# Optimization experiments

Hardware: AMD Instinct MI355X
Metric: run time of the kernel (lower is better)

## Reference

```python
import jax, jax.numpy as jnp
import numpy as np

N0, N1, N2 = 409600, 40960, 4096
K = 10          # sampled fanout per dst node
IN, HID, NCLS = 512, 128, 64

def setup_inputs() -> dict:
    key = jax.random.key(0)
    ks = jax.random.split(key, 11)
    return {
        "embed":   jax.random.normal(ks[0], (N0, IN), jnp.float32),
        "h0_hist": jax.random.normal(ks[1], (N0, IN), jnp.float32),
        "h1_hist": jax.random.normal(ks[2], (N1, 2 * HID), jnp.float32),
        "agg_h0":  jax.random.normal(ks[3], (N1, IN), jnp.float32),
        "agg_h1":  jax.random.normal(ks[4], (N2, 2 * HID), jnp.float32),
        "W1": jax.random.normal(ks[5], (IN, HID), jnp.float32) / np.sqrt(IN),
        "b1": jax.random.normal(ks[6], (HID,), jnp.float32) * 0.01,
        "W2": jax.random.normal(ks[7], (2 * HID, NCLS), jnp.float32) / np.sqrt(2 * HID),
        "b2": jax.random.normal(ks[8], (NCLS,), jnp.float32) * 0.01,
        "nbr0": jax.random.randint(ks[9], (N1, K), 0, N0, jnp.int64),
        "nbr1": jax.random.randint(ks[10], (N2, K), 0, N1, jnp.int64),
    }

def reference(embed, h0_hist, h1_hist, agg_h0, agg_h1, W1, b1, W2, b2, nbr0, nbr1):
    # ---- block 0 (training branch): history correction + mean aggregation ----
    h = embed - h0_hist                      # [N0, IN]
    agg = jnp.mean(h[nbr0], axis=1)          # gather [N1, K, IN] -> mean -> [N1, IN]
    h = agg + agg_h0                         # add aggregated history (agg_h_0)
    h = h @ W1 + b1                          # dense [N1, HID]
    h = jnp.concatenate([h, jax.nn.relu(h)], axis=1)  # concat (skip_start) -> [N1, 2*HID]
    # ---- block 1: history correction + mean aggregation + final dense ----
    h = h - h1_hist                          # [N1, 2*HID]
    agg = jnp.mean(h[nbr1], axis=1)          # [N2, 2*HID]
    h = agg + agg_h1
    h = h @ W2 + b2                          # [N2, NCLS], no activation on last layer
    return h
```

## Files before the change

kernel.cpp:

```cpp
#include <hip/hip_runtime.h>
#include <stdint.h>

#define N0 409600
#define N1 40960
#define N2 4096
#define KF 10
#define IN 512
#define HID 128
#define NCLS 64
#define NB 16

static __device__ __forceinline__ float4 f4_zero() { return make_float4(0.f, 0.f, 0.f, 0.f); }

#define GATHER5x2(d0,d1,d2,d3,d4,d5,d6,d7,d8,d9, o0,o1,o2,o3,o4, base)      \
    asm volatile(                                                            \
        "global_load_dwordx4 %0, %10, %15 offset:0\n\t"                      \
        "global_load_dwordx4 %1, %10, %15 offset:16\n\t"                     \
        "global_load_dwordx4 %2, %11, %15 offset:0\n\t"                      \
        "global_load_dwordx4 %3, %11, %15 offset:16\n\t"                     \
        "global_load_dwordx4 %4, %12, %15 offset:0\n\t"                      \
        "global_load_dwordx4 %5, %12, %15 offset:16\n\t"                     \
        "global_load_dwordx4 %6, %13, %15 offset:0\n\t"                      \
        "global_load_dwordx4 %7, %13, %15 offset:16\n\t"                     \
        "global_load_dwordx4 %8, %14, %15 offset:0\n\t"                      \
        "global_load_dwordx4 %9, %14, %15 offset:16\n\t"                     \
        "s_waitcnt vmcnt(0)"                                                 \
        : "=&v"(d0), "=&v"(d1), "=&v"(d2), "=&v"(d3), "=&v"(d4),             \
          "=&v"(d5), "=&v"(d6), "=&v"(d7), "=&v"(d8), "=&v"(d9)              \
        : "v"(o0), "v"(o1), "v"(o2), "v"(o3), "v"(o4), "s"(base)             \
        : "memory")

#define GATHER10x1(d0,d1,d2,d3,d4,d5,d6,d7,d8,d9,                            \
                   o0,o1,o2,o3,o4,o5,o6,o7,o8,o9, base)                      \
    asm volatile(                                                            \
        "global_load_dwordx4 %0, %10, %20 offset:0\n\t"                      \
        "global_load_dwordx4 %1, %11, %20 offset:0\n\t"                      \
        "global_load_dwordx4 %2, %12, %20 offset:0\n\t"                      \
        "global_load_dwordx4 %3, %13, %20 offset:0\n\t"                      \
        "global_load_dwordx4 %4, %14, %20 offset:0\n\t"                      \
        "global_load_dwordx4 %5, %15, %20 offset:0\n\t"                      \
        "global_load_dwordx4 %6, %16, %20 offset:0\n\t"                      \
        "global_load_dwordx4 %7, %17, %20 offset:0\n\t"                      \
        "global_load_dwordx4 %8, %18, %20 offset:0\n\t"                      \
        "global_load_dwordx4 %9, %19, %20 offset:0\n\t"                      \
        "s_waitcnt vmcnt(0)"                                                 \
        : "=&v"(d0), "=&v"(d1), "=&v"(d2), "=&v"(d3), "=&v"(d4),             \
          "=&v"(d5), "=&v"(d6), "=&v"(d7), "=&v"(d8), "=&v"(d9)              \
        : "v"(o0), "v"(o1), "v"(o2), "v"(o3), "v"(o4),                       \
          "v"(o5), "v"(o6), "v"(o7), "v"(o8), "v"(o9), "s"(base)             \
        : "memory")

__global__ __launch_bounds__(256) void k_block0(
    const float* __restrict__ embed, const float* __restrict__ h0_hist,
    const float* __restrict__ h1_hist, const float* __restrict__ agg_h0,
    const float* __restrict__ W1, const float* __restrict__ b1,
    const int* __restrict__ nbr0, float* __restrict__ h1p)
{
    __shared__ float A[NB][IN];
    const int t = threadIdx.x;
    const int wave = t >> 6;
    const int lane = t & 63;
    const int base_node = blockIdx.x * NB;

    const uint64_t be = (uint64_t)embed;
    const uint64_t bg = (uint64_t)h0_hist;
    const uint32_t lane_byte = (uint32_t)lane * 32u;

    #pragma unroll 1
    for (int i = 0; i < NB / 4; ++i) {
        const int nl = wave * (NB / 4) + i;
        const int node = base_node + nl;
        const int nb = node * KF;
        float4 acc0 = f4_zero(), acc1 = f4_zero();

        int idx[KF];
        #pragma unroll
        for (int j = 0; j < KF; ++j) idx[j] = nbr0[nb + j];

        #pragma unroll 1
        for (int c = 0; c < 2; ++c) {
            uint32_t v0 = (uint32_t)idx[c * 5 + 0] * (uint32_t)(IN * 4) + lane_byte;
            uint32_t v1 = (uint32_t)idx[c * 5 + 1] * (uint32_t)(IN * 4) + lane_byte;
            uint32_t v2 = (uint32_t)idx[c * 5 + 2] * (uint32_t)(IN * 4) + lane_byte;
            uint32_t v3 = (uint32_t)idx[c * 5 + 3] * (uint32_t)(IN * 4) + lane_byte;
            uint32_t v4 = (uint32_t)idx[c * 5 + 4] * (uint32_t)(IN * 4) + lane_byte;

            float4 e0, e1, e2, e3, e4, e5, e6, e7, e8, e9;
            GATHER5x2(e0, e1, e2, e3, e4, e5, e6, e7, e8, e9,
                      v0, v1, v2, v3, v4, be);
            acc0.x += e0.x + e2.x + e4.x + e6.x + e8.x;
            acc0.y += e0.y + e2.y + e4.y + e6.y + e8.y;
            acc0.z += e0.z + e2.z + e4.z + e6.z + e8.z;
            acc0.w += e0.w + e2.w + e4.w + e6.w + e8.w;
            acc1.x += e1.x + e3.x + e5.x + e7.x + e9.x;
            acc1.y += e1.y + e3.y + e5.y + e7.y + e9.y;
            acc1.z += e1.z + e3.z + e5.z + e7.z + e9.z;
            acc1.w += e1.w + e3.w + e5.w + e7.w + e9.w;

            float4 g0, g1, g2, g3, g4, g5, g6, g7, g8, g9;
            GATHER5x2(g0, g1, g2, g3, g4, g5, g6, g7, g8, g9,
                      v0, v1, v2, v3, v4, bg);
            acc0.x -= g0.x + g2.x + g4.x + g6.x + g8.x;
            acc0.y -= g0.y + g2.y + g4.y + g6.y + g8.y;
            acc0.z -= g0.z + g2.z + g4.z + g6.z + g8.z;
            acc0.w -= g0.w + g2.w + g4.w + g6.w + g8.w;
            acc1.x -= g1.x + g3.x + g5.x + g7.x + g9.x;
            acc1.y -= g1.y + g3.y + g5.y + g7.y + g9.y;
            acc1.z -= g1.z + g3.z + g5.z + g7.z + g9.z;
            acc1.w -= g1.w + g3.w + g5.w + g7.w + g9.w;
        }

        const float s = 1.0f / (float)KF;
        const int col = lane * 8;
        const float4* ah = (const float4*)(agg_h0 + (size_t)node * IN + col);
        const float4 a0 = ah[0], a1 = ah[1];
        float4 r0, r1;
        r0.x = acc0.x * s + a0.x; r0.y = acc0.y * s + a0.y;
        r0.z = acc0.z * s + a0.z; r0.w = acc0.w * s + a0.w;
        r1.x = acc1.x * s + a1.x; r1.y = acc1.y * s + a1.y;
        r1.z = acc1.z * s + a1.z; r1.w = acc1.w * s + a1.w;
        *(float4*)&A[nl][col]     = r0;
        *(float4*)&A[nl][col + 4] = r1;
    }
    __syncthreads();

    const int c0 = (t & 31) * 4;
    const int rg = t >> 5;
    float4 acc[2];
    acc[0] = f4_zero(); acc[1] = f4_zero();

    #pragma unroll 4
    for (int k = 0; k < IN; ++k) {
        const float4 w = *(const float4*)&W1[k * HID + c0];
        #pragma unroll
        for (int i = 0; i < 2; ++i) {
            const float a = A[rg * 2 + i][k];
            acc[i].x += a * w.x; acc[i].y += a * w.y;
            acc[i].z += a * w.z; acc[i].w += a * w.w;
        }
    }

    const float4 bb = *(const float4*)&b1[c0];
    #pragma unroll
    for (int i = 0; i < 2; ++i) {
        const int node = base_node + rg * 2 + i;
        float4 h;
        h.x = acc[i].x + bb.x; h.y = acc[i].y + bb.y;
        h.z = acc[i].z + bb.z; h.w = acc[i].w + bb.w;
        const float4 hh0 = *(const float4*)&h1_hist[node * (2 * HID) + c0];
        const float4 hh1 = *(const float4*)&h1_hist[node * (2 * HID) + HID + c0];
        float4 o0, o1;
        o0.x = h.x - hh0.x; o0.y = h.y - hh0.y;
        o0.z = h.z - hh0.z; o0.w = h.w - hh0.w;
        o1.x = fmaxf(h.x, 0.f) - hh1.x; o1.y = fmaxf(h.y, 0.f) - hh1.y;
        o1.z = fmaxf(h.z, 0.f) - hh1.z; o1.w = fmaxf(h.w, 0.f) - hh1.w;
        *(float4*)&h1p[node * (2 * HID) + c0]       = o0;
        *(float4*)&h1p[node * (2 * HID) + HID + c0] = o1;
    }
}

__global__ __launch_bounds__(256) void k_block1(
    const float* __restrict__ h1p, const float* __restrict__ agg_h1,
    const float* __restrict__ W2, const float* __restrict__ b2,
    const int* __restrict__ nbr1, float* __restrict__ out)
{
    __shared__ float B[8][2 * HID + 4];
    const int t = threadIdx.x;
    const int wave = t >> 6;
    const int lane = t & 63;
    const int base_node = blockIdx.x * 8;
    const uint64_t bh = (uint64_t)h1p;
    const uint32_t lane_byte = (uint32_t)lane * 16u;

    #pragma unroll 1
    for (int i = 0; i < 2; ++i) {
        const int nl = wave * 2 + i;
        const int node = base_node + nl;
        const int nb = node * KF;

        uint32_t o[KF];
        #pragma unroll
        for (int j = 0; j < KF; ++j)
            o[j] = (uint32_t)nbr1[nb + j] * (uint32_t)(2 * HID * 4) + lane_byte;

        float4 v0, v1, v2, v3, v4, v5, v6, v7, v8, v9;
        GATHER10x1(v0, v1, v2, v3, v4, v5, v6, v7, v8, v9,
                   o[0], o[1], o[2], o[3], o[4],
                   o[5], o[6], o[7], o[8], o[9], bh);

        float4 acc;
        acc.x = v0.x + v1.x + v2.x + v3.x + v4.x + v5.x + v6.x + v7.x + v8.x + v9.x;
        acc.y = v0.y + v1.y + v2.y + v3.y + v4.y + v5.y + v6.y + v7.y + v8.y + v9.y;
        acc.z = v0.z + v1.z + v2.z + v3.z + v4.z + v5.z + v6.z + v7.z + v8.z + v9.z;
        acc.w = v0.w + v1.w + v2.w + v3.w + v4.w + v5.w + v6.w + v7.w + v8.w + v9.w;

        const float s = 1.0f / (float)KF;
        const int col = lane * 4;
        const float4 g = *(const float4*)&agg_h1[(size_t)node * (2 * HID) + col];
        float4 r;
        r.x = acc.x * s + g.x; r.y = acc.y * s + g.y;
        r.z = acc.z * s + g.z; r.w = acc.w * s + g.w;
        *(float4*)&B[nl][col] = r;
    }
    __syncthreads();

    const int r = t >> 5;
    const int c0 = (t & 31) * 2;
    float2 acc = make_float2(0.f, 0.f);
    #pragma unroll 4
    for (int k = 0; k < 2 * HID; ++k) {
        const float a = B[r][k];
        const float2 w = *(const float2*)&W2[k * NCLS + c0];
        acc.x += a * w.x; acc.y += a * w.y;
    }
    const float2 bb = *(const float2*)&b2[c0];
    float2 o;
    o.x = acc.x + bb.x; o.y = acc.y + bb.y;
    const int node = base_node + r;
    *(float2*)&out[node * NCLS + c0] = o;
}

extern "C" void kernel_launch(void* const* d_in, const int* in_sizes, int n_in,
                              void* d_out, int out_size, void* d_ws, size_t ws_size,
                              hipStream_t stream) {
    const float* embed   = (const float*)d_in[0];
    const float* h0_hist = (const float*)d_in[1];
    const float* h1_hist = (const float*)d_in[2];
    const float* agg_h0  = (const float*)d_in[3];
    const float* agg_h1  = (const float*)d_in[4];
    const float* W1      = (const float*)d_in[5];
    const float* b1      = (const float*)d_in[6];
    const float* W2      = (const float*)d_in[7];
    const float* b2      = (const float*)d_in[8];
    const int*   nbr0    = (const int*)d_in[9];
    const int*   nbr1    = (const int*)d_in[10];
    float* out = (float*)d_out;

    float* h1p = (float*)d_ws;

    k_block0<<<N1 / NB, 256, 0, stream>>>(embed, h0_hist, h1_hist, agg_h0,
                                          W1, b1, nbr0, h1p);
    k_block1<<<N2 / 8, 256, 0, stream>>>(h1p, agg_h1, W2, b2, nbr1, out);
}
```

Before: 442.4 us.

## Split block-0 gather and dense into separate kernels with wider gather batches

The fused block-0 kernel is split in two. A gather kernel handles one node per wave, issues all 20 embed and history loads for five neighbours in a single batch, and writes the aggregated rows to a workspace buffer. A separate dense kernel reloads those rows into shared memory for the W1 matmul. This is meant to raise memory-level parallelism and occupancy for the gather and keep the latency-bound gather from serialising with the GEMM. The cost is an extra round trip of an 80 MB intermediate through global memory and one more launch.

```diff
diff --git a/kernel.cpp b/kernel.cpp
--- a/kernel.cpp
+++ b/kernel.cpp
@@ -8,26 +8,39 @@
 #define IN 512
 #define HID 128
 #define NCLS 64
-#define NB 16
 
 static __device__ __forceinline__ float4 f4_zero() { return make_float4(0.f, 0.f, 0.f, 0.f); }
 
-#define GATHER5x2(d0,d1,d2,d3,d4,d5,d6,d7,d8,d9, o0,o1,o2,o3,o4, base)      \
+#define GATHER20(E0,H0,G0,F0, E1,H1,G1,F1, E2,H2,G2,F2, E3,H3,G3,F3,         \
+                 E4,H4,G4,F4, o0,o1,o2,o3,o4, be, bg)                        \
     asm volatile(                                                            \
-        "global_load_dwordx4 %0, %10, %15 offset:0\n\t"                      \
-        "global_load_dwordx4 %1, %10, %15 offset:16\n\t"                     \
-        "global_load_dwordx4 %2, %11, %15 offset:0\n\t"                      \
-        "global_load_dwordx4 %3, %11, %15 offset:16\n\t"                     \
-        "global_load_dwordx4 %4, %12, %15 offset:0\n\t"                      \
-        "global_load_dwordx4 %5, %12, %15 offset:16\n\t"                     \
-        "global_load_dwordx4 %6, %13, %15 offset:0\n\t"                      \
-        "global_load_dwordx4 %7, %13, %15 offset:16\n\t"                     \
-        "global_load_dwordx4 %8, %14, %15 offset:0\n\t"                      \
-        "global_load_dwordx4 %9, %14, %15 offset:16\n\t"                     \
+        "global_load_dwordx4 %0, %20, %25 offset:0\n\t"                      \
+        "global_load_dwordx4 %1, %20, %25 offset:16\n\t"                     \
+        "global_load_dwordx4 %2, %20, %26 offset:0\n\t"                      \
+        "global_load_dwordx4 %3, %20, %26 offset:16\n\t"                     \
+        "global_load_dwordx4 %4, %21, %25 offset:0\n\t"                      \
+        "global_load_dwordx4 %5, %21, %25 offset:16\n\t"                     \
+        "global_load_dwordx4 %6, %21, %26 offset:0\n\t"                      \
+        "global_load_dwordx4 %7, %21, %26 offset:16\n\t"                     \
+        "global_load_dwordx4 %8, %22, %25 offset:0\n\t"                      \
+        "global_load_dwordx4 %9, %22, %25 offset:16\n\t"                     \
+        "global_load_dwordx4 %10, %22, %26 offset:0\n\t"                     \
+        "global_load_dwordx4 %11, %22, %26 offset:16\n\t"                    \
+        "global_load_dwordx4 %12, %23, %25 offset:0\n\t"                     \
+        "global_load_dwordx4 %13, %23, %25 offset:16\n\t"                    \
+        "global_load_dwordx4 %14, %23, %26 offset:0\n\t"                     \
+        "global_load_dwordx4 %15, %23, %26 offset:16\n\t"                    \
+        "global_load_dwordx4 %16, %24, %25 offset:0\n\t"                     \
+        "global_load_dwordx4 %17, %24, %25 offset:16\n\t"                    \
+        "global_load_dwordx4 %18, %24, %26 offset:0\n\t"                     \
+        "global_load_dwordx4 %19, %24, %26 offset:16\n\t"                    \
         "s_waitcnt vmcnt(0)"                                                 \
-        : "=&v"(d0), "=&v"(d1), "=&v"(d2), "=&v"(d3), "=&v"(d4),             \
-          "=&v"(d5), "=&v"(d6), "=&v"(d7), "=&v"(d8), "=&v"(d9)              \
-        : "v"(o0), "v"(o1), "v"(o2), "v"(o3), "v"(o4), "s"(base)             \
+        : "=&v"(E0), "=&v"(H0), "=&v"(G0), "=&v"(F0),                        \
+          "=&v"(E1), "=&v"(H1), "=&v"(G1), "=&v"(F1),                        \
+          "=&v"(E2), "=&v"(H2), "=&v"(G2), "=&v"(F2),                        \
+          "=&v"(E3), "=&v"(H3), "=&v"(G3), "=&v"(F3),                        \
+          "=&v"(E4), "=&v"(H4), "=&v"(G4), "=&v"(F4)                         \
+        : "v"(o0), "v"(o1), "v"(o2), "v"(o3), "v"(o4), "s"(be), "s"(bg)      \
         : "memory")
 
 #define GATHER10x1(d0,d1,d2,d3,d4,d5,d6,d7,d8,d9,                            \
@@ -50,77 +63,79 @@
           "v"(o5), "v"(o6), "v"(o7), "v"(o8), "v"(o9), "s"(base)             \
         : "memory")
 
-__global__ __launch_bounds__(256) void k_block0(
+__global__ __launch_bounds__(256) void k_gather0(
     const float* __restrict__ embed, const float* __restrict__ h0_hist,
-    const float* __restrict__ h1_hist, const float* __restrict__ agg_h0,
-    const float* __restrict__ W1, const float* __restrict__ b1,
-    const int* __restrict__ nbr0, float* __restrict__ h1p)
+    const float* __restrict__ agg_h0, const int* __restrict__ nbr0,
+    float* __restrict__ aggbuf)
 {
-    __shared__ float A[NB][IN];
     const int t = threadIdx.x;
     const int wave = t >> 6;
     const int lane = t & 63;
-    const int base_node = blockIdx.x * NB;
-
+    const int node = blockIdx.x * 4 + wave;
+    const int nb = node * KF;
     const uint64_t be = (uint64_t)embed;
     const uint64_t bg = (uint64_t)h0_hist;
     const uint32_t lane_byte = (uint32_t)lane * 32u;
 
+    float4 acc0 = f4_zero(), acc1 = f4_zero();
+
+    int idx[KF];
+    #pragma unroll
+    for (int j = 0; j < KF; ++j) idx[j] = nbr0[nb + j];
+
     #pragma unroll 1
-    for (int i = 0; i < NB / 4; ++i) {
-        const int nl = wave * (NB / 4) + i;
-        const int node = base_node + nl;
-        const int nb = node * KF;
-        float4 acc0 = f4_zero(), acc1 = f4_zero();
-
-        int idx[KF];
-        #pragma unroll
-        for (int j = 0; j < KF; ++j) idx[j] = nbr0[nb + j];
-
-        #pragma unroll 1
-        for (int c = 0; c < 2; ++c) {
-            uint32_t v0 = (uint32_t)idx[c * 5 + 0] * (uint32_t)(IN * 4) + lane_byte;
-            uint32_t v1 = (uint32_t)idx[c * 5 + 1] * (uint32_t)(IN * 4) + lane_byte;
-            uint32_t v2 = (uint32_t)idx[c * 5 + 2] * (uint32_t)(IN * 4) + lane_byte;
-            uint32_t v3 = (uint32_t)idx[c * 5 + 3] * (uint32_t)(IN * 4) + lane_byte;
-            uint32_t v4 = (uint32_t)idx[c * 5 + 4] * (uint32_t)(IN * 4) + lane_byte;
-
-            float4 e0, e1, e2, e3, e4, e5, e6, e7, e8, e9;
-            GATHER5x2(e0, e1, e2, e3, e4, e5, e6, e7, e8, e9,
-                      v0, v1, v2, v3, v4, be);
-            acc0.x += e0.x + e2.x + e4.x + e6.x + e8.x;
-            acc0.y += e0.y + e2.y + e4.y + e6.y + e8.y;
-            acc0.z += e0.z + e2.z + e4.z + e6.z + e8.z;
-            acc0.w += e0.w + e2.w + e4.w + e6.w + e8.w;
-            acc1.x += e1.x + e3.x + e5.x + e7.x + e9.x;
-            acc1.y += e1.y + e3.y + e5.y + e7.y + e9.y;
-            acc1.z += e1.z + e3.z + e5.z + e7.z + e9.z;
-            acc1.w += e1.w + e3.w + e5.w + e7.w + e9.w;
-
-            float4 g0, g1, g2, g3, g4, g5, g6, g7, g8, g9;
-            GATHER5x2(g0, g1, g2, g3, g4, g5, g6, g7, g8, g9,
-                      v0, v1, v2, v3, v4, bg);
-            acc0.x -= g0.x + g2.x + g4.x + g6.x + g8.x;
-            acc0.y -= g0.y + g2.y + g4.y + g6.y + g8.y;
-            acc0.z -= g0.z + g2.z + g4.z + g6.z + g8.z;
-            acc0.w -= g0.w + g2.w + g4.w + g6.w + g8.w;
-            acc1.x -= g1.x + g3.x + g5.x + g7.x + g9.x;
-            acc1.y -= g1.y + g3.y + g5.y + g7.y + g9.y;
-            acc1.z -= g1.z + g3.z + g5.z + g7.z + g9.z;
-            acc1.w -= g1.w + g3.w + g5.w + g7.w + g9.w;
-        }
-
-        const float s = 1.0f / (float)KF;
-        const int col = lane * 8;
-        const float4* ah = (const float4*)(agg_h0 + (size_t)node * IN + col);
-        const float4 a0 = ah[0], a1 = ah[1];
-        float4 r0, r1;
-        r0.x = acc0.x * s + a0.x; r0.y = acc0.y * s + a0.y;
-        r0.z = acc0.z * s + a0.z; r0.w = acc0.w * s + a0.w;
-        r1.x = acc1.x * s + a1.x; r1.y = acc1.y * s + a1.y;
-        r1.z = acc1.z * s + a1.z; r1.w = acc1.w * s + a1.w;
-        *(float4*)&A[nl][col]     = r0;
-        *(float4*)&A[nl][col + 4] = r1;
+    for (int c = 0; c < 2; ++c) {
+        const uint32_t v0 = (uint32_t)idx[c * 5 + 0] * (uint32_t)(IN * 4) + lane_byte;
+        const uint32_t v1 = (uint32_t)idx[c * 5 + 1] * (uint32_t)(IN * 4) + lane_byte;
+        const uint32_t v2 = (uint32_t)idx[c * 5 + 2] * (uint32_t)(IN * 4) + lane_byte;
+        const uint32_t v3 = (uint32_t)idx[c * 5 + 3] * (uint32_t)(IN * 4) + lane_byte;
+        const uint32_t v4 = (uint32_t)idx[c * 5 + 4] * (uint32_t)(IN * 4) + lane_byte;
+
+        float4 E0, H0, G0, F0, E1, H1, G1, F1, E2, H2, G2, F2,
+               E3, H3, G3, F3, E4, H4, G4, F4;
+        GATHER20(E0, H0, G0, F0, E1, H1, G1, F1, E2, H2, G2, F2,
+                 E3, H3, G3, F3, E4, H4, G4, F4,
+                 v0, v1, v2, v3, v4, be, bg);
+
+        acc0.x += (E0.x + E1.x + E2.x + E3.x + E4.x) - (G0.x + G1.x + G2.x + G3.x + G4.x);
+        acc0.y += (E0.y + E1.y + E2.y + E3.y + E4.y) - (G0.y + G1.y + G2.y + G3.y + G4.y);
+        acc0.z += (E0.z + E1.z + E2.z + E3.z + E4.z) - (G0.z + G1.z + G2.z + G3.z + G4.z);
+        acc0.w += (E0.w + E1.w + E2.w + E3.w + E4.w) - (G0.w + G1.w + G2.w + G3.w + G4.w);
+        acc1.x += (H0.x + H1.x + H2.x + H3.x + H4.x) - (F0.x + F1.x + F2.x + F3.x + F4.x);
+        acc1.y += (H0.y + H1.y + H2.y + H3.y + H4.y) - (F0.y + F1.y + F2.y + F3.y + F4.y);
+        acc1.z += (H0.z + H1.z + H2.z + H3.z + H4.z) - (F0.z + F1.z + F2.z + F3.z + F4.z);
+        acc1.w += (H0.w + H1.w + H2.w + H3.w + H4.w) - (F0.w + F1.w + F2.w + F3.w + F4.w);
+    }
+
+    const float s = 1.0f / (float)KF;
+    const int col = lane * 8;
+    const float4* ah = (const float4*)(agg_h0 + (size_t)node * IN + col);
+    const float4 a0 = ah[0], a1 = ah[1];
+    float4 r0, r1;
+    r0.x = acc0.x * s + a0.x; r0.y = acc0.y * s + a0.y;
+    r0.z = acc0.z * s + a0.z; r0.w = acc0.w * s + a0.w;
+    r1.x = acc1.x * s + a1.x; r1.y = acc1.y * s + a1.y;
+    r1.z = acc1.z * s + a1.z; r1.w = acc1.w * s + a1.w;
+    *(float4*)&aggbuf[(size_t)node * IN + col]     = r0;
+    *(float4*)&aggbuf[(size_t)node * IN + col + 4] = r1;
+}
+
+__global__ __launch_bounds__(256) void k_dense0(
+    const float* __restrict__ aggbuf, const float* __restrict__ h1_hist,
+    const float* __restrict__ W1, const float* __restrict__ b1,
+    float* __restrict__ h1p)
+{
+    __shared__ float A[16][IN];
+    const int t = threadIdx.x;
+    const int base_node = blockIdx.x * 16;
+
+    const int r2 = t >> 7;
+    const int c4 = (t & 127) * 4;
+    #pragma unroll
+    for (int rr = 0; rr < 8; ++rr) {
+        const int row = rr * 2 + r2;
+        *(float4*)&A[row][c4] =
+            *(const float4*)&aggbuf[(size_t)(base_node + row) * IN + c4];
     }
     __syncthreads();
 
@@ -236,9 +251,10 @@
     const int*   nbr1    = (const int*)d_in[10];
     float* out = (float*)d_out;
 
-    float* h1p = (float*)d_ws;
-
-    k_block0<<<N1 / NB, 256, 0, stream>>>(embed, h0_hist, h1_hist, agg_h0,
-                                          W1, b1, nbr0, h1p);
+    float* aggbuf = (float*)d_ws;
+    float* h1p    = aggbuf + (size_t)N1 * IN;
+
+    k_gather0<<<N1 / 4, 256, 0, stream>>>(embed, h0_hist, agg_h0, nbr0, aggbuf);
+    k_dense0<<<N1 / 16, 256, 0, stream>>>(aggbuf, h1_hist, W1, b1, h1p);
     k_block1<<<N2 / 8, 256, 0, stream>>>(h1p, agg_h1, W2, b2, nbr1, out);
 }
```

Measured after the change: 551.8 us. 24.7% more time.
